# Kernel tuning notes

Hardware: AMD Instinct MI355X
Metric: run time of the kernel (lower is better)

## Reference

```python
import jax, jax.numpy as jnp
import numpy as np

STEPS = 2
P_TOPP = 0.9
TAU = 1.0
LN_EPS = 1e-5


def _top_p_attention(pooled, W1, W2, W3):
    # pooled: (N, C). Bilinear scores -> softmax -> nucleus (top-p) sparsify -> renorm.
    e1 = pooled @ W1.T                      # (N, d)
    e3 = pooled @ W3.T                      # (N, d)
    logits = (e1 @ W2.T) @ e3.T / TAU       # (N, N)
    attn = jax.nn.softmax(logits, axis=-1)
    srt = jnp.sort(attn, axis=-1)[:, ::-1]  # descending
    csum = jnp.cumsum(srt, axis=-1)
    keep = (csum - srt) < P_TOPP            # keep entries whose exclusive cum-prob < p
    thr = jnp.min(jnp.where(keep, srt, jnp.inf), axis=-1, keepdims=True)
    masked = jnp.where(attn >= thr, attn, 0.0)
    return masked / jnp.clip(jnp.sum(masked, axis=-1, keepdims=True), 1e-12)


def _layernorm(h, gamma, beta):
    mu = jnp.mean(h, axis=-1, keepdims=True)
    var = jnp.mean(jnp.square(h - mu), axis=-1, keepdims=True)
    return (h - mu) * jax.lax.rsqrt(var + LN_EPS) * gamma + beta


def _forward(x, prior, W1, W2, W3, prior_fwd_w, adaptive_w, ln_gamma, ln_beta, alpha):
    # Row-normalised prior (forward diffusion operator)
    Rf = prior / jnp.clip(jnp.sum(prior, axis=1, keepdims=True), 1e-12)
    Xf = x
    Xa = x
    residual = jnp.zeros_like(x)
    for idx in range(STEPS):
        pooled = jnp.mean(Xa, axis=1)                      # protein axis pooling -> (N_P, C)
        attn = _top_p_attention(pooled, W1, W2, W3)        # (N_P, N_P)
        Xf = jnp.einsum('ij,jkc->ikc', Rf, Xf)
        Xa = jnp.einsum('ij,jkc->ikc', attn, Xa)
        delta = jnp.einsum('ikc,dc->ikd', Xf, prior_fwd_w[idx]) \
              + jnp.einsum('ikc,dc->ikd', Xa, adaptive_w[idx])
        residual = residual + delta                        # dropout is identity in eval mode
    gate = jax.nn.sigmoid(alpha)                           # (1,)
    return _layernorm(x + gate * residual, ln_gamma, ln_beta)


def setup_inputs() -> dict:
    key = jax.random.key(0)
    ks = jax.random.split(key, 8)
    N_P, N_C, C, D = 2048, 64, 128, 64
    x = jax.random.normal(ks[0], (N_P, N_C, C), dtype=jnp.float32)
    prior = jax.random.uniform(ks[1], (N_P, N_P), dtype=jnp.float32)
    W1 = jax.random.normal(ks[2], (D, C), dtype=jnp.float32) / np.sqrt(C)
    W2 = jax.random.normal(ks[3], (D, D), dtype=jnp.float32) / np.sqrt(D)
    W3 = jax.random.normal(ks[4], (D, C), dtype=jnp.float32) / np.sqrt(C)
    prior_fwd_w = jax.random.normal(ks[5], (STEPS, C, C), dtype=jnp.float32) / np.sqrt(C)
    adaptive_w = jax.random.normal(ks[6], (STEPS, C, C), dtype=jnp.float32) / np.sqrt(C)
    ln_gamma = jnp.ones((C,), dtype=jnp.float32)
    ln_beta = jnp.zeros((C,), dtype=jnp.float32)
    alpha = jnp.zeros((1,), dtype=jnp.float32)
    return {"x": x, "prior": prior, "W1": W1, "W2": W2, "W3": W3,
            "prior_fwd_w": prior_fwd_w, "adaptive_w": adaptive_w,
            "ln_gamma": ln_gamma, "ln_beta": ln_beta, "alpha": alpha}


def reference(x, prior, W1, W2, W3, prior_fwd_w, adaptive_w, ln_gamma, ln_beta, alpha):
    return _forward(x, prior, W1, W2, W3, prior_fwd_w, adaptive_w, ln_gamma, ln_beta, alpha)
```

## Files before the change

### kernel.cpp

```cpp
#include <hip/hip_runtime.h>

typedef unsigned short u16;
typedef __attribute__((ext_vector_type(8))) short short8;
typedef __attribute__((ext_vector_type(4))) float f32x4;
typedef __attribute__((ext_vector_type(16))) float f32x16;

#define AS1 __attribute__((address_space(1)))
#define AS3 __attribute__((address_space(3)))

__device__ __forceinline__ void async_cp16(const void* g, void* l) {
  __builtin_amdgcn_global_load_lds((const AS1 unsigned int*)g, (AS3 unsigned int*)l, 16, 0, 0);
}

__device__ __forceinline__ u16 f2bf(float f) {
  union { float f; unsigned u; } v; v.f = f;
  unsigned r = v.u + 0x7fffu + ((v.u >> 16) & 1u);
  return (u16)(r >> 16);
}
__device__ __forceinline__ float bf2f(u16 h) {
  union { unsigned u; float f; } v; v.u = ((unsigned)h) << 16;
  return v.f;
}

template<int MODE>
__global__ __launch_bounds__(256, 2) void gemm32(
    const u16* __restrict__ A, const u16* __restrict__ B,
    int M, int N, int K,
    u16* __restrict__ Crow, int crow_ld, int crow_coloff,
    u16* __restrict__ Ct, int ct_ld)
{
  __shared__ u16 smem[12288];
  u16* sA = smem;
  u16* sB = smem + 4096;
  const int tid  = threadIdx.x;
  const int lane = tid & 63;
  const int wid  = tid >> 6;
  const int m0 = blockIdx.y * 128;
  const int n0 = blockIdx.x * 256;
  const int wm = (wid >> 1) * 64;
  const int wn = (wid & 1) * 128;
  const int l31  = lane & 31;
  const int half = lane >> 5;
  const int pl   = (l31 & 3) ^ ((l31 >> 2) & 3);

  f32x16 acc[2][4];
#pragma unroll
  for (int i = 0; i < 2; i++)
#pragma unroll
    for (int j = 0; j < 4; j++)
#pragma unroll
      for (int r = 0; r < 16; r++) acc[i][j][r] = 0.f;

  const int r4 = tid >> 2;
  const int cc = tid & 3;
  const int g8 = (cc ^ ((r4 & 3) ^ ((r4 >> 2) & 3))) * 8;
  const u16* gA0 = A + (size_t)(m0 + r4) * K + g8;
  const u16* gA1 = A + (size_t)(m0 + 64 + r4) * K + g8;
  const u16* gB0 = B + (size_t)(n0 + r4) * K + g8;
  const u16* gB1 = B + (size_t)(n0 + 64 + r4) * K + g8;
  const u16* gB2 = B + (size_t)(n0 + 128 + r4) * K + g8;
  const u16* gB3 = B + (size_t)(n0 + 192 + r4) * K + g8;
  u16* lA0 = sA + wid * 512;
  u16* lA1 = sA + 2048 + wid * 512;
  u16* lB0 = sB + wid * 512;
  u16* lB1 = sB + 2048 + wid * 512;
  u16* lB2 = sB + 4096 + wid * 512;
  u16* lB3 = sB + 6144 + wid * 512;

  for (int k0 = 0; k0 < K; k0 += 32) {
    async_cp16(gA0 + k0, lA0);
    async_cp16(gA1 + k0, lA1);
    async_cp16(gB0 + k0, lB0);
    async_cp16(gB1 + k0, lB1);
    async_cp16(gB2 + k0, lB2);
    async_cp16(gB3 + k0, lB3);
    __syncthreads();
#pragma unroll
    for (int s = 0; s < 2; s++) {
      const int kc = ((s * 2 + half) ^ pl) * 8;
      short8 aF[2], bF[4];
#pragma unroll
      for (int i = 0; i < 2; i++)
        aF[i] = *(const short8*)(sA + (wm + i * 32 + l31) * 32 + kc);
#pragma unroll
      for (int j = 0; j < 4; j++)
        bF[j] = *(const short8*)(sB + (wn + j * 32 + l31) * 32 + kc);
#pragma unroll
      for (int i = 0; i < 2; i++)
#pragma unroll
        for (int j = 0; j < 4; j++)
          acc[i][j] = __builtin_amdgcn_mfma_f32_32x32x16_bf16(aF[i], bF[j], acc[i][j], 0, 0, 0);
    }
    __syncthreads();
  }

  u16* T = smem;

#pragma unroll
  for (int pr = 0; pr < 2; pr++)
#pragma unroll
    for (int pc = 0; pc < 2; pc++) {
      if (((wid >> 1) == pr) && ((wid & 1) == pc)) {
#pragma unroll
        for (int i = 0; i < 2; i++)
#pragma unroll
          for (int j = 0; j < 4; j++)
#pragma unroll
            for (int r = 0; r < 16; r++) {
              const int rrow = i * 32 + (r & 3) + 8 * (r >> 2) + 4 * half;
              T[rrow * 136 + j * 32 + l31] = f2bf(acc[i][j][r]);
            }
      }
      __syncthreads();
      {
        const int row = tid >> 2, q = tid & 3;
        const size_t crow = (size_t)(m0 + pr * 64 + row) * (N >> 7) + (n0 >> 7) + pc;
        u16* dst = Crow + crow * (size_t)crow_ld + crow_coloff + q * 32;
        const u16* src = T + row * 136 + q * 32;
#pragma unroll
        for (int u = 0; u < 4; u++) ((float4*)dst)[u] = ((const float4*)src)[u];
      }
      __syncthreads();
    }

  if constexpr (MODE == 1) {
#pragma unroll
    for (int p = 0; p < 4; p++) {
      if ((wid & 1) == (p >> 1)) {
        const int jb = (p & 1) * 2;
#pragma unroll
        for (int i = 0; i < 2; i++)
#pragma unroll
          for (int jj = 0; jj < 2; jj++)
#pragma unroll
            for (int r = 0; r < 16; r++) {
              const int nloc = jj * 32 + l31;
              const int mcol = wm + i * 32 + (r & 3) + 8 * (r >> 2) + 4 * half;
              T[nloc * 136 + mcol] = f2bf(acc[i][jb + jj][r]);
            }
      }
      __syncthreads();
      {
        const int row = tid >> 2, q = tid & 3;
        u16* dst = Ct + (size_t)(n0 + p * 64 + row) * ct_ld + m0 + q * 32;
        const u16* src = T + row * 136 + q * 32;
#pragma unroll
        for (int u = 0; u < 4; u++) ((float4*)dst)[u] = ((const float4*)src)[u];
      }
      __syncthreads();
    }
  }
}

template<int MODE>
__global__ __launch_bounds__(256) void gemm_bt(
    const u16* __restrict__ A, const u16* __restrict__ B,
    int M, int N, int K,
    float* __restrict__ Cf,
    u16* __restrict__ Crow, int crow_ld, int crow_coloff)
{
  extern __shared__ char smemc[];
  u16* sA = (u16*)smemc;
  u16* sB = (u16*)(smemc + 8192);
  const int tid  = threadIdx.x;
  const int lane = tid & 63;
  const int wid  = tid >> 6;
  const int m0 = blockIdx.y * 128;
  const int n0 = blockIdx.x * 128;
  const int wm = (wid >> 1) * 64;
  const int wn = (wid & 1) * 64;
  const int ml = lane & 15;
  const int qd = lane >> 4;

  f32x4 acc[4][4];
  const f32x4 zero = {0.f, 0.f, 0.f, 0.f};
#pragma unroll
  for (int i = 0; i < 4; i++)
#pragma unroll
    for (int j = 0; j < 4; j++) acc[i][j] = zero;

  const int r4 = tid >> 2;
  const int c4 = (tid & 3) * 8;
  const u16* gA0 = A + (size_t)(m0 + r4) * K + c4;
  const u16* gA1 = A + (size_t)(m0 + 64 + r4) * K + c4;
  const u16* gB0 = B + (size_t)(n0 + r4) * K + c4;
  const u16* gB1 = B + (size_t)(n0 + 64 + r4) * K + c4;
  u16* lA0 = sA + wid * 512;
  u16* lA1 = sA + 2048 + wid * 512;
  u16* lB0 = sB + wid * 512;
  u16* lB1 = sB + 2048 + wid * 512;

  for (int k0 = 0; k0 < K; k0 += 32) {
    async_cp16(gA0 + k0, lA0);
    async_cp16(gA1 + k0, lA1);
    async_cp16(gB0 + k0, lB0);
    async_cp16(gB1 + k0, lB1);
    __syncthreads();
    short8 af[4], bfr[4];
#pragma unroll
    for (int i = 0; i < 4; i++)
      af[i] = *(const short8*)(sA + (wm + i * 16 + ml) * 32 + qd * 8);
#pragma unroll
    for (int j = 0; j < 4; j++)
      bfr[j] = *(const short8*)(sB + (wn + j * 16 + ml) * 32 + qd * 8);
#pragma unroll
    for (int i = 0; i < 4; i++)
#pragma unroll
      for (int j = 0; j < 4; j++)
        acc[i][j] = __builtin_amdgcn_mfma_f32_16x16x32_bf16(af[i], bfr[j], acc[i][j], 0, 0, 0);
    __syncthreads();
  }

  if constexpr (MODE == 3) {
#pragma unroll
    for (int i = 0; i < 4; i++) {
      const int mr = m0 + wm + i * 16 + qd * 4;
#pragma unroll
      for (int j = 0; j < 4; j++) {
        const int nc = n0 + wn + j * 16 + ml;
        float* p = Cf + (size_t)mr * N + nc;
#pragma unroll
        for (int r = 0; r < 4; r++) p[(size_t)r * N] = acc[i][j][r];
      }
    }
  } else {
    u16* T = (u16*)smemc;
#pragma unroll
    for (int i = 0; i < 4; i++)
#pragma unroll
      for (int j = 0; j < 4; j++)
#pragma unroll
        for (int r = 0; r < 4; r++)
          T[(wm + i * 16 + qd * 4 + r) * 136 + wn + j * 16 + ml] = f2bf(acc[i][j][r]);
    __syncthreads();
    const int row = tid >> 1, halfr = tid & 1;
    const size_t crow = (size_t)(m0 + row) * (N >> 7) + (n0 >> 7);
    u16* dst = Crow + crow * (size_t)crow_ld + crow_coloff + halfr * 64;
    const u16* src = T + row * 136 + halfr * 64;
#pragma unroll
    for (int u = 0; u < 8; u++) ((float4*)dst)[u] = ((const float4*)src)[u];
  }
}

__global__ void rowsum_k(const float* __restrict__ prior, float* __restrict__ rs) {
  const int i = blockIdx.x, t = threadIdx.x;
  const float* p = prior + (size_t)i * 2048;
  float s = 0.f;
  for (int j = t; j < 2048; j += 256) s += p[j];
  __shared__ float red[256];
  red[t] = s; __syncthreads();
  for (int o = 128; o; o >>= 1) { if (t < o) red[t] += red[t + o]; __syncthreads(); }
  if (t == 0) rs[i] = red[0];
}

__global__ void convprior_k(const float4* __restrict__ prior, const float* __restrict__ rs,
                            ushort4* __restrict__ dst) {
  const int idx = blockIdx.x * 256 + threadIdx.x;
  const float inv = 1.0f / rs[idx >> 9];
  const float4 v = prior[idx];
  ushort4 o;
  o.x = f2bf(v.x * inv); o.y = f2bf(v.y * inv); o.z = f2bf(v.z * inv); o.w = f2bf(v.w * inv);
  dst[idx] = o;
}

__global__ void convx_k(const float* __restrict__ x, u16* __restrict__ xt) {
  __shared__ float S[64][65];
  const int t = threadIdx.x;
  const int j0 = blockIdx.y * 64;
  const int n0 = blockIdx.x * 64;
  const int rr = t >> 4, cxc = (t & 15) * 4;
#pragma unroll
  for (int p = 0; p < 4; p++) {
    const float4 v = *(const float4*)(x + (size_t)(j0 + rr + p * 16) * 8192 + n0 + cxc);
    S[rr + p * 16][cxc + 0] = v.x; S[rr + p * 16][cxc + 1] = v.y;
    S[rr + p * 16][cxc + 2] = v.z; S[rr + p * 16][cxc + 3] = v.w;
  }
  __syncthreads();
  const int nl = t >> 2, ch = (t & 3) * 16;
  alignas(16) u16 tmp[16];
#pragma unroll
  for (int u = 0; u < 16; u++) tmp[u] = f2bf(S[ch + u][nl]);
  float4* dst = (float4*)(xt + (size_t)(n0 + nl) * 2048 + j0 + ch);
  dst[0] = ((const float4*)tmp)[0];
  dst[1] = ((const float4*)tmp)[1];
}

__global__ void convw_k(const float* __restrict__ pw, const float* __restrict__ aw,
                        u16* __restrict__ btc) {
  const int idx = blockIdx.x * 256 + threadIdx.x;
  const int k = idx & 255, d = (idx >> 8) & 127, s = idx >> 15;
  const float v = (k < 128) ? aw[(s * 128 + d) * 128 + k] : pw[(s * 128 + d) * 128 + (k - 128)];
  btc[idx] = f2bf(v);
}

__global__ void pooled1_k(const float* __restrict__ x, float* __restrict__ pooled) {
  const int i = blockIdx.x, t = threadIdx.x;
  const int c = t & 127, h = t >> 7;
  const float* base = x + (size_t)i * 8192 + c;
  float s = 0.f;
  for (int k = h * 32; k < h * 32 + 32; k++) s += base[(size_t)k * 128];
  __shared__ float red[256];
  red[t] = s; __syncthreads();
  if (t < 128) pooled[i * 128 + t] = (red[t] + red[t + 128]) * (1.f / 64.f);
}

__global__ void pooled2_k(const u16* __restrict__ comb, float* __restrict__ pooled) {
  const int i = blockIdx.x, t = threadIdx.x;
  const int c = t & 127, h = t >> 7;
  const u16* base = comb + (size_t)i * 64 * 256 + c;
  float s = 0.f;
  for (int k = h * 32; k < h * 32 + 32; k++) s += bf2f(base[(size_t)k * 256]);
  __shared__ float red[256];
  red[t] = s; __syncthreads();
  if (t < 128) pooled[i * 128 + t] = (red[t] + red[t + 128]) * (1.f / 64.f);
}

__global__ void epre_k(const float* __restrict__ pooled,
                       const float* __restrict__ W1, const float* __restrict__ W2,
                       const float* __restrict__ W3,
                       u16* __restrict__ e3b, u16* __restrict__ fb) {
  const int i = blockIdx.x, d = threadIdx.x;
  __shared__ float pr[128], e1s[64];
  pr[d] = pooled[i * 128 + d];
  pr[d + 64] = pooled[i * 128 + 64 + d];
  __syncthreads();
  float s1 = 0.f, s3 = 0.f;
  for (int c = 0; c < 128; c++) {
    const float p = pr[c];
    s1 += p * W1[d * 128 + c];
    s3 += p * W3[d * 128 + c];
  }
  e1s[d] = s1;
  e3b[i * 64 + d] = f2bf(s3);
  __syncthreads();
  float sf = 0.f;
  for (int dd = 0; dd < 64; dd++) sf += e1s[dd] * W2[d * 64 + dd];
  fb[i * 64 + d] = f2bf(sf);
}

__device__ __forceinline__ float waveRedSum(float v) {
#pragma unroll
  for (int o = 1; o < 64; o <<= 1) v += __shfl_xor(v, o);
  return __shfl(v, 0);
}
__device__ __forceinline__ float waveRedMax(float v) {
#pragma unroll
  for (int o = 1; o < 64; o <<= 1) v = fmaxf(v, __shfl_xor(v, o));
  return __shfl(v, 0);
}

__global__ __launch_bounds__(256) void topp_k(const float* __restrict__ logits,
                                              u16* __restrict__ attnb) {
  const int w = threadIdx.x >> 6, l = threadIdx.x & 63;
  const int i = blockIdx.x * 4 + w;
  const float4* row = (const float4*)(logits + (size_t)i * 2048);
  float E[32];
  float mx = -1e30f;
#pragma unroll
  for (int k = 0; k < 8; k++) {
    const float4 v = row[k * 64 + l];
    E[k * 4 + 0] = v.x; E[k * 4 + 1] = v.y; E[k * 4 + 2] = v.z; E[k * 4 + 3] = v.w;
    mx = fmaxf(fmaxf(mx, fmaxf(v.x, v.y)), fmaxf(v.z, v.w));
  }
  mx = waveRedMax(mx);
  float S = 0.f;
#pragma unroll
  for (int u = 0; u < 32; u++) { E[u] = __expf(E[u] - mx); S += E[u]; }
  S = waveRedSum(S);
  const float target = 0.9f * S;
  float lo = 0.f, hi = 1.f;
  for (int it = 0; it < 32; ++it) {
    const float mid = 0.5f * (lo + hi);
    float g = 0.f;
#pragma unroll
    for (int u = 0; u < 32; u++) g += (E[u] > mid) ? E[u] : 0.f;
    g = waveRedSum(g);
    const bool below = (g < target);
    hi = below ? mid : hi;
    lo = below ? lo : mid;
  }
  float Sk = 0.f;
#pragma unroll
  for (int u = 0; u < 32; u++) Sk += (E[u] > lo) ? E[u] : 0.f;
  Sk = waveRedSum(Sk);
  const float inv = 1.f / Sk;
  u16* dst = attnb + (size_t)i * 2048;
#pragma unroll
  for (int k = 0; k < 8; k++) {
    ushort4 o;
    o.x = f2bf(E[k * 4 + 0] > lo ? E[k * 4 + 0] * inv : 0.f);
    o.y = f2bf(E[k * 4 + 1] > lo ? E[k * 4 + 1] * inv : 0.f);
    o.z = f2bf(E[k * 4 + 2] > lo ? E[k * 4 + 2] * inv : 0.f);
    o.w = f2bf(E[k * 4 + 3] > lo ? E[k * 4 + 3] * inv : 0.f);
    *(ushort4*)(dst + k * 256 + l * 4) = o;
  }
}

__global__ void ln_k(const float* __restrict__ x,
                     const u16* __restrict__ d1, const u16* __restrict__ d2,
                     float* __restrict__ out,
                     const float* __restrict__ gamma, const float* __restrict__ beta,
                     const float* __restrict__ alpha) {
  const int wid = threadIdx.x >> 6, lane = threadIdx.x & 63;
  const float gate = 1.f / (1.f + expf(-alpha[0]));
  const float2 g = ((const float2*)gamma)[lane];
  const float2 b = ((const float2*)beta)[lane];
#pragma unroll
  for (int rr = 0; rr < 2; ++rr) {
    const size_t row = (size_t)blockIdx.x * 8 + wid * 2 + rr;
    const float2 xv = ((const float2*)(x + row * 128))[lane];
    const ushort2 r1 = ((const ushort2*)(d1 + row * 128))[lane];
    const ushort2 r2 = ((const ushort2*)(d2 + row * 128))[lane];
    const float h0 = xv.x + gate * (bf2f(r1.x) + bf2f(r2.x));
    const float h1 = xv.y + gate * (bf2f(r1.y) + bf2f(r2.y));
    float s = h0 + h1;
#pragma unroll
    for (int o = 32; o; o >>= 1) s += __shfl_down(s, o);
    const float mu = __shfl(s, 0) * (1.f / 128.f);
    const float d0 = h0 - mu, dd1 = h1 - mu;
    float vs = d0 * d0 + dd1 * dd1;
#pragma unroll
    for (int o = 32; o; o >>= 1) vs += __shfl_down(vs, o);
    const float rstd = rsqrtf(__shfl(vs, 0) * (1.f / 128.f) + 1e-5f);
    float2* op = (float2*)(out + row * 128);
    float2 ov;
    ov.x = d0 * rstd * g.x + b.x;
    ov.y = dd1 * rstd * g.y + b.y;
    op[lane] = ov;
  }
}

extern "C" void kernel_launch(void* const* d_in, const int* in_sizes, int n_in,
                              void* d_out, int out_size, void* d_ws, size_t ws_size,
                              hipStream_t stream) {
  const float* x     = (const float*)d_in[0];
  const float* prior = (const float*)d_in[1];
  const float* W1    = (const float*)d_in[2];
  const float* W2    = (const float*)d_in[3];
  const float* W3    = (const float*)d_in[4];
  const float* Pw    = (const float*)d_in[5];
  const float* Aw    = (const float*)d_in[6];
  const float* gamma = (const float*)d_in[7];
  const float* beta  = (const float*)d_in[8];
  const float* alpha = (const float*)d_in[9];
  float* out = (float*)d_out;

  char* w = (char*)d_ws;
  u16*   Xt_x   = (u16*)(w);
  u16*   XtA    = (u16*)(w + 33554432);
  u16*   XtF    = (u16*)(w + 67108864);
  u16*   comb   = (u16*)(w + 100663296);
  u16*   priorS = (u16*)(w + 167772160);
  u16*   attnb  = (u16*)(w + 176160768);
  float* pooled = (float*)(w + 184549376);
  u16*   e3b    = (u16*)(w + 185597952);
  u16*   fb     = (u16*)(w + 186122240);
  float* rs     = (float*)(w + 186646528);
  u16*   btc    = (u16*)(w + 186654720);
  float* logits1 = (float*)(w + 33554432);
  float* logits2 = (float*)(w);
  u16*   d1      = (u16*)(w);
  u16*   d2      = (u16*)(w + 33554432);
  (void)in_sizes; (void)n_in; (void)ws_size;

  rowsum_k   <<<2048, 256, 0, stream>>>(prior, rs);
  convprior_k<<<4096, 256, 0, stream>>>((const float4*)prior, rs, (ushort4*)priorS);
  convx_k    <<<dim3(128, 32), 256, 0, stream>>>(x, Xt_x);
  convw_k    <<<256, 256, 0, stream>>>(Pw, Aw, btc);

  pooled1_k  <<<2048, 256, 0, stream>>>(x, pooled);
  epre_k     <<<2048, 64, 0, stream>>>(pooled, W1, W2, W3, e3b, fb);
  gemm_bt<3> <<<dim3(16, 16), 256, 16384, stream>>>(fb, e3b, 2048, 2048, 64,
                                                    logits1, nullptr, 0, 0);
  topp_k     <<<512, 256, 0, stream>>>(logits1, attnb);

  gemm32<1><<<dim3(32, 16), 256, 0, stream>>>(attnb,  Xt_x, 2048, 8192, 2048,
                                              comb, 256, 0,   XtA, 2048);
  gemm32<1><<<dim3(32, 16), 256, 0, stream>>>(priorS, Xt_x, 2048, 8192, 2048,
                                              comb, 256, 128, XtF, 2048);

  pooled2_k  <<<2048, 256, 0, stream>>>(comb, pooled);
  epre_k     <<<2048, 64, 0, stream>>>(pooled, W1, W2, W3, e3b, fb);
  gemm_bt<3> <<<dim3(16, 16), 256, 16384, stream>>>(fb, e3b, 2048, 2048, 64,
                                                    logits2, nullptr, 0, 0);
  topp_k     <<<512, 256, 0, stream>>>(logits2, attnb);

  gemm_bt<2><<<dim3(1, 1024), 256, 34816, stream>>>(comb, btc, 131072, 128, 256,
                                                    nullptr, d1, 128, 0);

  gemm32<2><<<dim3(32, 16), 256, 0, stream>>>(attnb,  XtA, 2048, 8192, 2048,
                                              comb, 256, 0,   nullptr, 0);
  gemm32<2><<<dim3(32, 16), 256, 0, stream>>>(priorS, XtF, 2048, 8192, 2048,
                                              comb, 256, 128, nullptr, 0);

  gemm_bt<2><<<dim3(1, 1024), 256, 34816, stream>>>(comb, btc + 32768, 131072, 128, 256,
                                                    nullptr, d2, 128, 0);

  ln_k<<<16384, 256, 0, stream>>>(x, d1, d2, out, gamma, beta, alpha);
}
```

Before: 686.8 us.

## Enlarge diffusion GEMM tile to 256x256 with 4-stage async LDS pipeline

Rewrites the main bf16 diffusion GEMM to use 512-thread blocks computing 256x256 tiles, with a 4-deep ring of LDS buffers filled by async global-to-LDS loads and explicit vmcnt waits, so loads for later K-steps overlap MFMA work. It also raises wave priority around the MFMA bursts and widens the epilogue stores. The aim is to cut global traffic per FLOP and hide load latency that the old single-buffered loop exposed at every K-step. In exchange it uses 128 KB of dynamic LDS per block, which limits occupancy to one block per CU, and it launches half as many blocks.

```diff
diff --git a/kernel.cpp b/kernel.cpp
--- a/kernel.cpp
+++ b/kernel.cpp
@@ -23,127 +23,149 @@
 }
 
 template<int MODE>
-__global__ __launch_bounds__(256, 2) void gemm32(
+__global__ __launch_bounds__(512, 2) void gemm32(
     const u16* __restrict__ A, const u16* __restrict__ B,
     int M, int N, int K,
     u16* __restrict__ Crow, int crow_ld, int crow_coloff,
     u16* __restrict__ Ct, int ct_ld)
 {
-  __shared__ u16 smem[12288];
-  u16* sA = smem;
-  u16* sB = smem + 4096;
+  extern __shared__ u16 smem[];
   const int tid  = threadIdx.x;
   const int lane = tid & 63;
-  const int wid  = tid >> 6;
-  const int m0 = blockIdx.y * 128;
+  const int w    = tid >> 6;
+  const int m0 = blockIdx.y * 256;
   const int n0 = blockIdx.x * 256;
-  const int wm = (wid >> 1) * 64;
-  const int wn = (wid & 1) * 128;
+  const int wm = w >> 2;
+  const int wn = w & 3;
   const int l31  = lane & 31;
   const int half = lane >> 5;
   const int pl   = (l31 & 3) ^ ((l31 >> 2) & 3);
 
-  f32x16 acc[2][4];
-#pragma unroll
-  for (int i = 0; i < 2; i++)
-#pragma unroll
-    for (int j = 0; j < 4; j++)
+  f32x16 acc[4][2];
+#pragma unroll
+  for (int i = 0; i < 4; i++)
+#pragma unroll
+    for (int j = 0; j < 2; j++)
 #pragma unroll
       for (int r = 0; r < 16; r++) acc[i][j][r] = 0.f;
 
-  const int r4 = tid >> 2;
-  const int cc = tid & 3;
-  const int g8 = (cc ^ ((r4 & 3) ^ ((r4 >> 2) & 3))) * 8;
-  const u16* gA0 = A + (size_t)(m0 + r4) * K + g8;
-  const u16* gA1 = A + (size_t)(m0 + 64 + r4) * K + g8;
-  const u16* gB0 = B + (size_t)(n0 + r4) * K + g8;
-  const u16* gB1 = B + (size_t)(n0 + 64 + r4) * K + g8;
-  const u16* gB2 = B + (size_t)(n0 + 128 + r4) * K + g8;
-  const u16* gB3 = B + (size_t)(n0 + 192 + r4) * K + g8;
-  u16* lA0 = sA + wid * 512;
-  u16* lA1 = sA + 2048 + wid * 512;
-  u16* lB0 = sB + wid * 512;
-  u16* lB1 = sB + 2048 + wid * 512;
-  u16* lB2 = sB + 4096 + wid * 512;
-  u16* lB3 = sB + 6144 + wid * 512;
-
-  for (int k0 = 0; k0 < K; k0 += 32) {
-    async_cp16(gA0 + k0, lA0);
-    async_cp16(gA1 + k0, lA1);
-    async_cp16(gB0 + k0, lB0);
-    async_cp16(gB1 + k0, lB1);
-    async_cp16(gB2 + k0, lB2);
-    async_cp16(gB3 + k0, lB3);
-    __syncthreads();
-#pragma unroll
-    for (int s = 0; s < 2; s++) {
-      const int kc = ((s * 2 + half) ^ pl) * 8;
-      short8 aF[2], bF[4];
-#pragma unroll
-      for (int i = 0; i < 2; i++)
-        aF[i] = *(const short8*)(sA + (wm + i * 32 + l31) * 32 + kc);
-#pragma unroll
-      for (int j = 0; j < 4; j++)
-        bF[j] = *(const short8*)(sB + (wn + j * 32 + l31) * 32 + kc);
-#pragma unroll
-      for (int i = 0; i < 2; i++)
-#pragma unroll
-        for (int j = 0; j < 4; j++)
+  const int sr = lane >> 2;
+  const int sc = lane & 3;
+  const int rA0 = w * 32 + sr;
+  const int rA1 = rA0 + 16;
+  const int pA0 = (rA0 & 3) ^ ((rA0 >> 2) & 3);
+  const int pA1 = (rA1 & 3) ^ ((rA1 >> 2) & 3);
+  const u16* gA0 = A + (size_t)(m0 + rA0) * K + (sc ^ pA0) * 8;
+  const u16* gA1 = A + (size_t)(m0 + rA1) * K + (sc ^ pA1) * 8;
+  const u16* gB0 = B + (size_t)(n0 + rA0) * K + (sc ^ pA0) * 8;
+  const u16* gB1 = B + (size_t)(n0 + rA1) * K + (sc ^ pA1) * 8;
+  const int stA0 = (w * 2 + 0) * 512;
+  const int stA1 = (w * 2 + 1) * 512;
+  const int stB0 = 8192 + stA0;
+  const int stB1 = 8192 + stA1;
+
+#define ISSUE(tt) do {                                   \
+    u16* sl = smem + ((tt) & 3) * 16384;                 \
+    const int ko = (tt) * 32;                            \
+    async_cp16(gA0 + ko, sl + stA0);                     \
+    async_cp16(gA1 + ko, sl + stA1);                     \
+    async_cp16(gB0 + ko, sl + stB0);                     \
+    async_cp16(gB1 + ko, sl + stB1);                     \
+  } while (0)
+
+  const int NT = K >> 5;
+  ISSUE(0); ISSUE(1); ISSUE(2);
+
+  for (int t = 0; t < NT; ++t) {
+    const int ahead = NT - 1 - t;
+    if (ahead >= 3) {
+      ISSUE(t + 3);
+      asm volatile("s_waitcnt vmcnt(12)" ::: "memory");
+    } else if (ahead == 2) {
+      asm volatile("s_waitcnt vmcnt(8)" ::: "memory");
+    } else if (ahead == 1) {
+      asm volatile("s_waitcnt vmcnt(4)" ::: "memory");
+    } else {
+      asm volatile("s_waitcnt vmcnt(0)" ::: "memory");
+    }
+    __builtin_amdgcn_s_barrier();
+    asm volatile("" ::: "memory");
+
+    const u16* sAp = smem + (t & 3) * 16384;
+    const u16* sBp = sAp + 8192;
+#pragma unroll
+    for (int ks = 0; ks < 2; ks++) {
+      const int kc = ((ks * 2 + half) ^ pl) * 8;
+      short8 aF[4], bF[2];
+#pragma unroll
+      for (int i = 0; i < 4; i++)
+        aF[i] = *(const short8*)(sAp + (wm * 128 + i * 32 + l31) * 32 + kc);
+#pragma unroll
+      for (int j = 0; j < 2; j++)
+        bF[j] = *(const short8*)(sBp + (wn * 64 + j * 32 + l31) * 32 + kc);
+      __builtin_amdgcn_s_setprio(1);
+#pragma unroll
+      for (int i = 0; i < 4; i++)
+#pragma unroll
+        for (int j = 0; j < 2; j++)
           acc[i][j] = __builtin_amdgcn_mfma_f32_32x32x16_bf16(aF[i], bF[j], acc[i][j], 0, 0, 0);
+      __builtin_amdgcn_s_setprio(0);
+    }
+
+    asm volatile("" ::: "memory");
+    __builtin_amdgcn_s_barrier();
+    asm volatile("" ::: "memory");
+  }
+#undef ISSUE
+
+  u16* T = smem;
+
+#pragma unroll
+  for (int pr = 0; pr < 4; pr++) {
+    if (wm == (pr >> 1)) {
+#pragma unroll
+      for (int ii = 0; ii < 2; ii++)
+#pragma unroll
+        for (int j = 0; j < 2; j++)
+#pragma unroll
+          for (int r = 0; r < 16; r++) {
+            const int rloc = ii * 32 + (r & 3) + 8 * (r >> 2) + 4 * half;
+            T[rloc * 264 + wn * 64 + j * 32 + l31] = f2bf(acc[(pr & 1) * 2 + ii][j][r]);
+          }
     }
     __syncthreads();
-  }
-
-  u16* T = smem;
-
-#pragma unroll
-  for (int pr = 0; pr < 2; pr++)
-#pragma unroll
-    for (int pc = 0; pc < 2; pc++) {
-      if (((wid >> 1) == pr) && ((wid & 1) == pc)) {
-#pragma unroll
-        for (int i = 0; i < 2; i++)
-#pragma unroll
-          for (int j = 0; j < 4; j++)
+    {
+      const int row = tid >> 3, c8 = tid & 7;
+      const size_t grow = (size_t)(m0 + pr * 64 + row);
+      const size_t crow = grow * (size_t)(N >> 7) + (n0 >> 7) + (c8 >> 2);
+      u16* dst = Crow + crow * (size_t)crow_ld + crow_coloff + (c8 & 3) * 32;
+      const u16* src = T + row * 264 + c8 * 32;
+#pragma unroll
+      for (int u = 0; u < 4; u++) ((float4*)dst)[u] = ((const float4*)src)[u];
+    }
+    __syncthreads();
+  }
+
+  if constexpr (MODE == 1) {
+#pragma unroll
+    for (int p = 0; p < 4; p++) {
+      if (wn == p) {
+#pragma unroll
+        for (int i = 0; i < 4; i++)
+#pragma unroll
+          for (int j = 0; j < 2; j++)
 #pragma unroll
             for (int r = 0; r < 16; r++) {
-              const int rrow = i * 32 + (r & 3) + 8 * (r >> 2) + 4 * half;
-              T[rrow * 136 + j * 32 + l31] = f2bf(acc[i][j][r]);
+              const int nloc = j * 32 + l31;
+              const int mcol = wm * 128 + i * 32 + (r & 3) + 8 * (r >> 2) + 4 * half;
+              T[nloc * 264 + mcol] = f2bf(acc[i][j][r]);
             }
       }
       __syncthreads();
       {
-        const int row = tid >> 2, q = tid & 3;
-        const size_t crow = (size_t)(m0 + pr * 64 + row) * (N >> 7) + (n0 >> 7) + pc;
-        u16* dst = Crow + crow * (size_t)crow_ld + crow_coloff + q * 32;
-        const u16* src = T + row * 136 + q * 32;
-#pragma unroll
-        for (int u = 0; u < 4; u++) ((float4*)dst)[u] = ((const float4*)src)[u];
-      }
-      __syncthreads();
-    }
-
-  if constexpr (MODE == 1) {
-#pragma unroll
-    for (int p = 0; p < 4; p++) {
-      if ((wid & 1) == (p >> 1)) {
-        const int jb = (p & 1) * 2;
-#pragma unroll
-        for (int i = 0; i < 2; i++)
-#pragma unroll
-          for (int jj = 0; jj < 2; jj++)
-#pragma unroll
-            for (int r = 0; r < 16; r++) {
-              const int nloc = jj * 32 + l31;
-              const int mcol = wm + i * 32 + (r & 3) + 8 * (r >> 2) + 4 * half;
-              T[nloc * 136 + mcol] = f2bf(acc[i][jb + jj][r]);
-            }
-      }
-      __syncthreads();
-      {
-        const int row = tid >> 2, q = tid & 3;
-        u16* dst = Ct + (size_t)(n0 + p * 64 + row) * ct_ld + m0 + q * 32;
-        const u16* src = T + row * 136 + q * 32;
+        const int row = tid >> 3, c8 = tid & 7;
+        u16* dst = Ct + (size_t)(n0 + p * 64 + row) * ct_ld + m0 + c8 * 32;
+        const u16* src = T + row * 264 + c8 * 32;
 #pragma unroll
         for (int u = 0; u < 4; u++) ((float4*)dst)[u] = ((const float4*)src)[u];
       }
@@ -463,6 +485,15 @@
   u16*   d2      = (u16*)(w + 33554432);
   (void)in_sizes; (void)n_in; (void)ws_size;
 
+  static bool attr_done = false;
+  if (!attr_done) {
+    hipFuncSetAttribute(reinterpret_cast<const void*>(gemm32<1>),
+                        hipFuncAttributeMaxDynamicSharedMemorySize, 131072);
+    hipFuncSetAttribute(reinterpret_cast<const void*>(gemm32<2>),
+                        hipFuncAttributeMaxDynamicSharedMemorySize, 131072);
+    attr_done = true;
+  }
+
   rowsum_k   <<<2048, 256, 0, stream>>>(prior, rs);
   convprior_k<<<4096, 256, 0, stream>>>((const float4*)prior, rs, (ushort4*)priorS);
   convx_k    <<<dim3(128, 32), 256, 0, stream>>>(x, Xt_x);
@@ -474,10 +505,10 @@
                                                     logits1, nullptr, 0, 0);
   topp_k     <<<512, 256, 0, stream>>>(logits1, attnb);
 
-  gemm32<1><<<dim3(32, 16), 256, 0, stream>>>(attnb,  Xt_x, 2048, 8192, 2048,
-                                              comb, 256, 0,   XtA, 2048);
-  gemm32<1><<<dim3(32, 16), 256, 0, stream>>>(priorS, Xt_x, 2048, 8192, 2048,
-                                              comb, 256, 128, XtF, 2048);
+  gemm32<1><<<dim3(32, 8), 512, 131072, stream>>>(attnb,  Xt_x, 2048, 8192, 2048,
+                                                  comb, 256, 0,   XtA, 2048);
+  gemm32<1><<<dim3(32, 8), 512, 131072, stream>>>(priorS, Xt_x, 2048, 8192, 2048,
+                                                  comb, 256, 128, XtF, 2048);
 
   pooled2_k  <<<2048, 256, 0, stream>>>(comb, pooled);
   epre_k     <<<2048, 64, 0, stream>>>(pooled, W1, W2, W3, e3b, fb);
@@ -488,10 +519,10 @@
   gemm_bt<2><<<dim3(1, 1024), 256, 34816, stream>>>(comb, btc, 131072, 128, 256,
                                                     nullptr, d1, 128, 0);
 
-  gemm32<2><<<dim3(32, 16), 256, 0, stream>>>(attnb,  XtA, 2048, 8192, 2048,
-                                              comb, 256, 0,   nullptr, 0);
-  gemm32<2><<<dim3(32, 16), 256, 0, stream>>>(priorS, XtF, 2048, 8192, 2048,
-                                              comb, 256, 128, nullptr, 0);
+  gemm32<2><<<dim3(32, 8), 512, 131072, stream>>>(attnb,  XtA, 2048, 8192, 2048,
+                                                  comb, 256, 0,   nullptr, 0);
+  gemm32<2><<<dim3(32, 8), 512, 131072, stream>>>(priorS, XtF, 2048, 8192, 2048,
+                                                  comb, 256, 128, nullptr, 0);
 
   gemm_bt<2><<<dim3(1, 1024), 256, 34816, stream>>>(comb, btc + 32768, 131072, 128, 256,
                                                     nullptr, d2, 128, 0);
```

Result: faster. 663.2 us (-3.4%).

## Merge paired diffusion GEMMs into one launch with 128x128 tiles and 16x16 MFMA

Applied to the files above, without the earlier changes.

The two separate 2048x8192x2048 GEMMs (attention branch and prior branch) are replaced by a single launch. The grid's y dimension now selects which branch each block computes. The block tile shrinks from 128x256 to 128x128, and the MFMA changes from 32x32x16 to 16x16x32. The launch-bounds occupancy hint and the XOR swizzle on LDS reads are dropped. The aim is more blocks in flight and fewer launches, at the risk of less operand reuse per block and LDS bank conflicts from the unswizzled layout.

```diff
diff --git a/kernel.cpp b/kernel.cpp
--- a/kernel.cpp
+++ b/kernel.cpp
@@ -3,7 +3,6 @@
 typedef unsigned short u16;
 typedef __attribute__((ext_vector_type(8))) short short8;
 typedef __attribute__((ext_vector_type(4))) float f32x4;
-typedef __attribute__((ext_vector_type(16))) float f32x16;
 
 #define AS1 __attribute__((address_space(1)))
 #define AS3 __attribute__((address_space(3)))
@@ -23,126 +22,112 @@
 }
 
 template<int MODE>
-__global__ __launch_bounds__(256, 2) void gemm32(
-    const u16* __restrict__ A, const u16* __restrict__ B,
-    int M, int N, int K,
-    u16* __restrict__ Crow, int crow_ld, int crow_coloff,
-    u16* __restrict__ Ct, int ct_ld)
+__global__ __launch_bounds__(256) void gemmF(
+    const u16* __restrict__ Aa, const u16* __restrict__ Ap,
+    const u16* __restrict__ Ba, const u16* __restrict__ Bp,
+    int K, int N,
+    u16* __restrict__ Crow, int crow_ld,
+    u16* __restrict__ Cta, u16* __restrict__ Ctp, int ct_ld)
 {
-  __shared__ u16 smem[12288];
-  u16* sA = smem;
-  u16* sB = smem + 4096;
+  extern __shared__ u16 smemf[];
+  u16* sA = smemf;
+  u16* sB = smemf + 4096;
   const int tid  = threadIdx.x;
   const int lane = tid & 63;
   const int wid  = tid >> 6;
-  const int m0 = blockIdx.y * 128;
-  const int n0 = blockIdx.x * 256;
+  const int half = blockIdx.y >> 4;
+  const int m0 = (blockIdx.y & 15) * 128;
+  const int n0 = blockIdx.x * 128;
+  const u16* A = half ? Ap : Aa;
+  const u16* B = half ? Bp : Ba;
+  const int coloff = half * 128;
   const int wm = (wid >> 1) * 64;
-  const int wn = (wid & 1) * 128;
-  const int l31  = lane & 31;
-  const int half = lane >> 5;
-  const int pl   = (l31 & 3) ^ ((l31 >> 2) & 3);
-
-  f32x16 acc[2][4];
-#pragma unroll
-  for (int i = 0; i < 2; i++)
-#pragma unroll
-    for (int j = 0; j < 4; j++)
-#pragma unroll
-      for (int r = 0; r < 16; r++) acc[i][j][r] = 0.f;
+  const int wn = (wid & 1) * 64;
+  const int ml = lane & 15;
+  const int qd = lane >> 4;
+
+  f32x4 acc[4][4];
+  const f32x4 zero = {0.f, 0.f, 0.f, 0.f};
+#pragma unroll
+  for (int i = 0; i < 4; i++)
+#pragma unroll
+    for (int j = 0; j < 4; j++) acc[i][j] = zero;
 
   const int r4 = tid >> 2;
-  const int cc = tid & 3;
-  const int g8 = (cc ^ ((r4 & 3) ^ ((r4 >> 2) & 3))) * 8;
-  const u16* gA0 = A + (size_t)(m0 + r4) * K + g8;
-  const u16* gA1 = A + (size_t)(m0 + 64 + r4) * K + g8;
-  const u16* gB0 = B + (size_t)(n0 + r4) * K + g8;
-  const u16* gB1 = B + (size_t)(n0 + 64 + r4) * K + g8;
-  const u16* gB2 = B + (size_t)(n0 + 128 + r4) * K + g8;
-  const u16* gB3 = B + (size_t)(n0 + 192 + r4) * K + g8;
+  const int c4 = (tid & 3) * 8;
+  const u16* gA0 = A + (size_t)(m0 + r4) * K + c4;
+  const u16* gA1 = A + (size_t)(m0 + 64 + r4) * K + c4;
+  const u16* gB0 = B + (size_t)(n0 + r4) * K + c4;
+  const u16* gB1 = B + (size_t)(n0 + 64 + r4) * K + c4;
   u16* lA0 = sA + wid * 512;
   u16* lA1 = sA + 2048 + wid * 512;
   u16* lB0 = sB + wid * 512;
   u16* lB1 = sB + 2048 + wid * 512;
-  u16* lB2 = sB + 4096 + wid * 512;
-  u16* lB3 = sB + 6144 + wid * 512;
 
   for (int k0 = 0; k0 < K; k0 += 32) {
     async_cp16(gA0 + k0, lA0);
     async_cp16(gA1 + k0, lA1);
     async_cp16(gB0 + k0, lB0);
     async_cp16(gB1 + k0, lB1);
-    async_cp16(gB2 + k0, lB2);
-    async_cp16(gB3 + k0, lB3);
-    __syncthreads();
-#pragma unroll
-    for (int s = 0; s < 2; s++) {
-      const int kc = ((s * 2 + half) ^ pl) * 8;
-      short8 aF[2], bF[4];
-#pragma unroll
-      for (int i = 0; i < 2; i++)
-        aF[i] = *(const short8*)(sA + (wm + i * 32 + l31) * 32 + kc);
+    __syncthreads();
+    short8 af[4], bfr[4];
+#pragma unroll
+    for (int i = 0; i < 4; i++)
+      af[i] = *(const short8*)(sA + (wm + i * 16 + ml) * 32 + qd * 8);
+#pragma unroll
+    for (int j = 0; j < 4; j++)
+      bfr[j] = *(const short8*)(sB + (wn + j * 16 + ml) * 32 + qd * 8);
+#pragma unroll
+    for (int i = 0; i < 4; i++)
 #pragma unroll
       for (int j = 0; j < 4; j++)
-        bF[j] = *(const short8*)(sB + (wn + j * 32 + l31) * 32 + kc);
-#pragma unroll
-      for (int i = 0; i < 2; i++)
+        acc[i][j] = __builtin_amdgcn_mfma_f32_16x16x32_bf16(af[i], bfr[j], acc[i][j], 0, 0, 0);
+    __syncthreads();
+  }
+
+  u16* T = smemf;
+
+#pragma unroll
+  for (int pr = 0; pr < 2; pr++) {
+    if ((wid >> 1) == pr) {
+#pragma unroll
+      for (int i = 0; i < 4; i++)
 #pragma unroll
         for (int j = 0; j < 4; j++)
-          acc[i][j] = __builtin_amdgcn_mfma_f32_32x32x16_bf16(aF[i], bF[j], acc[i][j], 0, 0, 0);
+#pragma unroll
+          for (int r = 0; r < 4; r++)
+            T[(i * 16 + qd * 4 + r) * 136 + wn + j * 16 + ml] = f2bf(acc[i][j][r]);
     }
     __syncthreads();
-  }
-
-  u16* T = smem;
-
-#pragma unroll
-  for (int pr = 0; pr < 2; pr++)
-#pragma unroll
-    for (int pc = 0; pc < 2; pc++) {
-      if (((wid >> 1) == pr) && ((wid & 1) == pc)) {
-#pragma unroll
-        for (int i = 0; i < 2; i++)
+    {
+      const int row = tid >> 2, q = tid & 3;
+      const size_t grow = (size_t)(m0 + pr * 64 + row);
+      const size_t crow = grow * (size_t)(N >> 7) + (n0 >> 7);
+      u16* dst = Crow + crow * (size_t)crow_ld + coloff + q * 32;
+      const u16* src = T + row * 136 + q * 32;
+#pragma unroll
+      for (int u = 0; u < 4; u++) ((float4*)dst)[u] = ((const float4*)src)[u];
+    }
+    __syncthreads();
+  }
+
+  if constexpr (MODE == 1) {
+    u16* Ct = half ? Ctp : Cta;
+#pragma unroll
+    for (int pt = 0; pt < 2; pt++) {
+      if ((wid & 1) == pt) {
+#pragma unroll
+        for (int i = 0; i < 4; i++)
 #pragma unroll
           for (int j = 0; j < 4; j++)
 #pragma unroll
-            for (int r = 0; r < 16; r++) {
-              const int rrow = i * 32 + (r & 3) + 8 * (r >> 2) + 4 * half;
-              T[rrow * 136 + j * 32 + l31] = f2bf(acc[i][j][r]);
-            }
+            for (int r = 0; r < 4; r++)
+              T[(j * 16 + ml) * 136 + wm + i * 16 + qd * 4 + r] = f2bf(acc[i][j][r]);
       }
       __syncthreads();
       {
         const int row = tid >> 2, q = tid & 3;
-        const size_t crow = (size_t)(m0 + pr * 64 + row) * (N >> 7) + (n0 >> 7) + pc;
-        u16* dst = Crow + crow * (size_t)crow_ld + crow_coloff + q * 32;
-        const u16* src = T + row * 136 + q * 32;
-#pragma unroll
-        for (int u = 0; u < 4; u++) ((float4*)dst)[u] = ((const float4*)src)[u];
-      }
-      __syncthreads();
-    }
-
-  if constexpr (MODE == 1) {
-#pragma unroll
-    for (int p = 0; p < 4; p++) {
-      if ((wid & 1) == (p >> 1)) {
-        const int jb = (p & 1) * 2;
-#pragma unroll
-        for (int i = 0; i < 2; i++)
-#pragma unroll
-          for (int jj = 0; jj < 2; jj++)
-#pragma unroll
-            for (int r = 0; r < 16; r++) {
-              const int nloc = jj * 32 + l31;
-              const int mcol = wm + i * 32 + (r & 3) + 8 * (r >> 2) + 4 * half;
-              T[nloc * 136 + mcol] = f2bf(acc[i][jb + jj][r]);
-            }
-      }
-      __syncthreads();
-      {
-        const int row = tid >> 2, q = tid & 3;
-        u16* dst = Ct + (size_t)(n0 + p * 64 + row) * ct_ld + m0 + q * 32;
+        u16* dst = Ct + (size_t)(n0 + pt * 64 + row) * ct_ld + m0 + q * 32;
         const u16* src = T + row * 136 + q * 32;
 #pragma unroll
         for (int u = 0; u < 4; u++) ((float4*)dst)[u] = ((const float4*)src)[u];
@@ -474,10 +459,9 @@
                                                     logits1, nullptr, 0, 0);
   topp_k     <<<512, 256, 0, stream>>>(logits1, attnb);
 
-  gemm32<1><<<dim3(32, 16), 256, 0, stream>>>(attnb,  Xt_x, 2048, 8192, 2048,
-                                              comb, 256, 0,   XtA, 2048);
-  gemm32<1><<<dim3(32, 16), 256, 0, stream>>>(priorS, Xt_x, 2048, 8192, 2048,
-                                              comb, 256, 128, XtF, 2048);
+  gemmF<1><<<dim3(64, 32), 256, 17408, stream>>>(attnb, priorS, Xt_x, Xt_x,
+                                                 2048, 8192, comb, 256,
+                                                 XtA, XtF, 2048);
 
   pooled2_k  <<<2048, 256, 0, stream>>>(comb, pooled);
   epre_k     <<<2048, 64, 0, stream>>>(pooled, W1, W2, W3, e3b, fb);
@@ -488,10 +472,9 @@
   gemm_bt<2><<<dim3(1, 1024), 256, 34816, stream>>>(comb, btc, 131072, 128, 256,
                                                     nullptr, d1, 128, 0);
 
-  gemm32<2><<<dim3(32, 16), 256, 0, stream>>>(attnb,  XtA, 2048, 8192, 2048,
-                                              comb, 256, 0,   nullptr, 0);
-  gemm32<2><<<dim3(32, 16), 256, 0, stream>>>(priorS, XtF, 2048, 8192, 2048,
-                                              comb, 256, 128, nullptr, 0);
+  gemmF<2><<<dim3(64, 32), 256, 17408, stream>>>(attnb, priorS, XtA, XtF,
+                                                 2048, 8192, comb, 256,
+                                                 nullptr, nullptr, 0);
 
   gemm_bt<2><<<dim3(1, 1024), 256, 34816, stream>>>(comb, btc + 32768, 131072, 128, 256,
                                                     nullptr, d2, 128, 0);
```

Result: slower. 731.8 us (+6.6%).
